# Kernel optimization log

Measured on AMD Instinct MI355X. Metric: run time of the kernel, lower is better.

The kernel has to match this reference:

```python
import jax, jax.numpy as jnp
import numpy as np

B, S, D, F, E, K, T = 4, 2048, 1024, 4096, 8, 2, 64


def setup_inputs() -> dict:
    key = jax.random.key(0)
    ks = jax.random.split(key, 12)
    s = 0.02
    return {
        "inputs": jax.random.normal(ks[0], (B, S, D), jnp.float32),
        "task_param": jax.random.normal(ks[1], (B, S, T), jnp.float32),
        "alpha": jnp.array(0.5, jnp.float32),
        "Wg_in": jax.random.normal(ks[2], (D, E), jnp.float32) * s,
        "bg_in": jnp.zeros((E,), jnp.float32),
        "Wg_task": jax.random.normal(ks[3], (T, E), jnp.float32) * s,
        "bg_task": jnp.zeros((E,), jnp.float32),
        "W1": jax.random.normal(ks[4], (E, D, F), jnp.float32) * s,
        "b1": jnp.zeros((E, F), jnp.float32),
        "W2": jax.random.normal(ks[5], (E, F, D), jnp.float32) * s,
        "b2": jnp.zeros((E, D), jnp.float32),
    }


def reference(inputs, task_param, alpha, Wg_in, bg_in, Wg_task, bg_task, W1, b1, W2, b2):
    dtype = inputs.dtype
    # blended gate logits: (1-alpha)*input_gate(x) + alpha*task_gate(task)
    gate_logits = (1.0 - alpha) * (jnp.einsum("bsd,de->bse", inputs, Wg_in) + bg_in) \
                + alpha * (jnp.einsum("bst,te->bse", task_param, Wg_task) + bg_task)
    # top-k expert selection (torch.topk: sorted descending)
    topk_vals, selected = jax.lax.top_k(gate_logits, K)  # [B,S,K]
    # aux load-balancing loss
    weights_softmax = jax.nn.softmax(gate_logits.astype(jnp.float32), axis=-1).astype(dtype)
    average_weight = weights_softmax.mean(axis=(0, 1))                 # [E]
    onehot = jax.nn.one_hot(selected, E, dtype=jnp.float32)            # [B,S,K,E]
    average_count = onehot.sum(axis=2).mean(axis=(0, 1)).astype(dtype) # [E]
    l_aux = jnp.mean(average_weight * average_count) * E
    # combine weights: softmax over the K selected logits, scattered to expert slots
    w = jax.nn.softmax(topk_vals.astype(jnp.float32), axis=-1).astype(dtype)  # [B,S,K]
    combine = jnp.einsum("bsk,bske->bse", w.astype(jnp.float32), onehot).astype(dtype)  # [B,S,E]
    # dense dispatch/combine (math-equivalent to boolean-mask gather/scatter loop)
    results = jnp.zeros_like(inputs)
    for e in range(E):
        h = jax.nn.gelu(jnp.einsum("bsd,df->bsf", inputs, W1[e]) + b1[e])
        y = jnp.einsum("bsf,fd->bsd", h, W2[e]) + b2[e]
        results = results + combine[..., e:e + 1] * y
    return (results, l_aux.astype(jnp.float32))
```

## Files before the change

kernel.cpp:

```cpp
#include <hip/hip_runtime.h>

#define NTOK 8192
#define DDIM 1024
#define FDIM 4096
#define NEXP 8
#define TDIM 64
#define MAXBLK 72

#define H_OFF   (1u<<20)
#define W1B_OFF (H_OFF + 134217728u)
#define W2B_OFF (W1B_OFF + 67108864u)
#define XB_OFF  (W2B_OFF + 67108864u)
#define FULL_WS (XB_OFF + 16777216u)
#define WS_BIG  (XB_OFF + 33554432u)

typedef __bf16 bf16x8 __attribute__((ext_vector_type(8)));
typedef unsigned short u16x8 __attribute__((ext_vector_type(8)));
typedef unsigned short u16x4 __attribute__((ext_vector_type(4)));
typedef float f32x4 __attribute__((ext_vector_type(4)));

__device__ __forceinline__ float gelu_tanh(float h) {
  float u = 0.7978845608028654f * (h + 0.044715f * h * h * h);
  float e = __expf(2.0f * u);
  return 0.5f * h * (2.0f - 2.0f / (e + 1.0f));
}

__device__ __forceinline__ void glds16(const void* g, void* l) {
  __builtin_amdgcn_global_load_lds((const __attribute__((address_space(1))) void*)g,
                                   (__attribute__((address_space(3))) void*)l, 16, 0, 0);
}

__global__ __launch_bounds__(256) void gate_kernel(
    const float* __restrict__ x, const float* __restrict__ task,
    const float* __restrict__ alpha_p,
    const float* __restrict__ Wg_in, const float* __restrict__ bg_in,
    const float* __restrict__ Wg_task, const float* __restrict__ bg_task,
    int* __restrict__ cnt, float* __restrict__ wsum,
    int* __restrict__ tok_list, float* __restrict__ wt_list)
{
  __shared__ float s_wsum[NEXP];
  int tid = threadIdx.x;
  if (tid < NEXP) s_wsum[tid] = 0.0f;
  __syncthreads();

  int lane = tid & 63;
  int wid  = tid >> 6;
  int tok  = blockIdx.x * 4 + wid;
  float a  = alpha_p[0];

  const float* xr = x + (size_t)tok * DDIM;
  float accd[8] = {0,0,0,0,0,0,0,0};
#pragma unroll
  for (int i = 0; i < DDIM/64; ++i) {
    int d = lane + 64*i;
    float xv = xr[d];
    f32x4 wa = *(const f32x4*)(Wg_in + (size_t)d*8);
    f32x4 wb = *(const f32x4*)(Wg_in + (size_t)d*8 + 4);
#pragma unroll
    for (int j = 0; j < 4; ++j) {
      accd[j]   = fmaf(xv, wa[j], accd[j]);
      accd[4+j] = fmaf(xv, wb[j], accd[4+j]);
    }
  }
  float part[8];
  {
    int d = lane;
    float tv = task[(size_t)tok*TDIM + d];
    f32x4 wa = *(const f32x4*)(Wg_task + (size_t)d*8);
    f32x4 wb = *(const f32x4*)(Wg_task + (size_t)d*8 + 4);
#pragma unroll
    for (int j = 0; j < 4; ++j) {
      part[j]   = (1.0f-a)*accd[j]   + a*(tv*wa[j]);
      part[4+j] = (1.0f-a)*accd[4+j] + a*(tv*wb[j]);
    }
  }
#pragma unroll
  for (int e = 0; e < 8; ++e) {
#pragma unroll
    for (int m = 1; m < 64; m <<= 1) part[e] += __shfl_xor(part[e], m);
  }

  if (lane == 0) {
    float lg[8];
#pragma unroll
    for (int e = 0; e < 8; ++e) lg[e] = part[e] + (1.0f-a)*bg_in[e] + a*bg_task[e];
    int e0 = 0;
#pragma unroll
    for (int e = 1; e < 8; ++e) if (lg[e] > lg[e0]) e0 = e;
    int e1 = (e0 == 0) ? 1 : 0;
#pragma unroll
    for (int e = 0; e < 8; ++e) if (e != e0 && lg[e] > lg[e1]) e1 = e;
    float mx = lg[0];
#pragma unroll
    for (int e = 1; e < 8; ++e) mx = fmaxf(mx, lg[e]);
    float p[8], s = 0.0f;
#pragma unroll
    for (int e = 0; e < 8; ++e) { p[e] = __expf(lg[e] - mx); s += p[e]; }
    float inv = 1.0f / s;
#pragma unroll
    for (int e = 0; e < 8; ++e) atomicAdd(&s_wsum[e], p[e] * inv);
    float p1 = __expf(lg[e1] - lg[e0]);
    float w0 = 1.0f / (1.0f + p1);
    float w1 = p1 * w0;
    int pos0 = atomicAdd(&cnt[e0], 1);
    tok_list[e0*NTOK + pos0] = tok; wt_list[e0*NTOK + pos0] = w0;
    int pos1 = atomicAdd(&cnt[e1], 1);
    tok_list[e1*NTOK + pos1] = tok; wt_list[e1*NTOK + pos1] = w1;
  }
  __syncthreads();
  if (tid < NEXP) atomicAdd(&wsum[tid], s_wsum[tid]);
}

__global__ void finalize_kernel(const int* __restrict__ cnt, const float* __restrict__ wsum,
                                int* __restrict__ offs, float* __restrict__ laux,
                                int* __restrict__ blk_e, int* __restrict__ blk_m)
{
  if (threadIdx.x == 0) {
    int o = 0; float l = 0.0f; int nb = 0;
    for (int e = 0; e < NEXP; ++e) {
      offs[e] = o;
      for (int m0 = 0; m0 < cnt[e]; m0 += 256) {
        if (nb < MAXBLK) { blk_e[nb] = e; blk_m[nb] = m0; ++nb; }
      }
      l += (wsum[e] * (1.0f/NTOK)) * ((float)cnt[e] * (1.0f/NTOK));
      o += cnt[e];
    }
    for (; nb < MAXBLK; ++nb) blk_e[nb] = -1;
    *laux = l;
  }
}

__global__ __launch_bounds__(256) void prep_x(const float* __restrict__ X,
                                              unsigned short* __restrict__ Xb)
{
  size_t i = ((size_t)blockIdx.x*256 + threadIdx.x)*8;
  f32x4 a = *(const f32x4*)(X + i);
  f32x4 b = *(const f32x4*)(X + i + 4);
  u16x8 v;
#pragma unroll
  for (int j = 0; j < 4; ++j) {
    v[j]   = __builtin_bit_cast(unsigned short, (__bf16)a[j]);
    v[4+j] = __builtin_bit_cast(unsigned short, (__bf16)b[j]);
  }
  *(u16x8*)(Xb + i) = v;
}

__global__ __launch_bounds__(256) void prep_gather(
    const float* __restrict__ X,
    const int* __restrict__ offs, const int* __restrict__ tok_list,
    unsigned short* __restrict__ Xg)
{
  int tid = threadIdx.x;
  int sl = blockIdx.x*2 + (tid >> 7);
  int e = 0;
#pragma unroll
  for (int k = 1; k < NEXP; ++k) if (sl >= offs[k]) e = k;
  int tok = tok_list[e*NTOK + (sl - offs[e])];
  int c8 = (tid & 127) * 8;
  const float* src = X + (size_t)tok * DDIM + c8;
  f32x4 a = *(const f32x4*)(src);
  f32x4 b = *(const f32x4*)(src + 4);
  u16x8 v;
#pragma unroll
  for (int j = 0; j < 4; ++j) {
    v[j]   = __builtin_bit_cast(unsigned short, (__bf16)a[j]);
    v[4+j] = __builtin_bit_cast(unsigned short, (__bf16)b[j]);
  }
  *(u16x8*)(Xg + (size_t)sl * DDIM + c8) = v;
}

template<bool PERM>
__global__ __launch_bounds__(256) void prep_w(const float* __restrict__ W,
                                              unsigned short* __restrict__ Wb,
                                              int N, int NKB, int NJ)
{
  int kb = blockIdx.x, J = blockIdx.y, e = blockIdx.z;
  int K = NKB*64;
  __shared__ unsigned short t[64*264];
  int tid = threadIdx.x;
  const float* src = W + ((size_t)e*K + (size_t)kb*64) * N + J*256;
  int k = tid >> 2, cg = tid & 3;
#pragma unroll
  for (int ii = 0; ii < 16; ++ii) {
    int n = cg*64 + ii*4;
    f32x4 v = *(const f32x4*)(src + (size_t)k*N + n);
    u16x4 b;
#pragma unroll
    for (int j = 0; j < 4; ++j) b[j] = __builtin_bit_cast(unsigned short, (__bf16)v[j]);
    *(u16x4*)&t[k*264 + n] = b;
  }
  __syncthreads();
  unsigned short* dst = Wb + ((size_t)(e*NJ + J)*NKB + kb)*16384;
#pragma unroll
  for (int i = 0; i < 8; ++i) {
    int c = i*256 + tid;
    int r = c >> 3, cc = c & 7;
    u16x8 v;
#pragma unroll
    for (int j = 0; j < 8; ++j) {
      int v64 = (cc ^ (r&7))*8 + j;
      int kl  = PERM ? (((v64 & 3) << 4) | (v64 >> 2)) : v64;
      v[j] = t[kl*264 + r];
    }
    *(u16x8*)(dst + c*8) = v;
  }
}


#define STAGE(sa, sb, ks) do {                                              \
  _Pragma("unroll")                                                         \
  for (int i_ = 0; i_ < 4; ++i_) {                                          \
    glds16(asrc[i_] + (size_t)(ks)*128, (char*)(sa) + dstoff[i_]);          \
    glds16(bsrc + (size_t)(ks)*32768 + i_*8192, (char*)(sb) + dstoff[i_]);  \
  }                                                                         \
} while (0)

#define COMPUTE(sa, sb) do {                                                \
  _Pragma("unroll")                                                         \
  for (int kk_ = 0; kk_ < 2; ++kk_) {                                       \
    int csw_ = ((kk_*4 + g) ^ (q & 7)) << 3;                                \
    bf16x8 bfv_[4];                                                         \
    _Pragma("unroll")                                                       \
    for (int ni_ = 0; ni_ < 4; ++ni_)                                       \
      bfv_[ni_] = *(const bf16x8*)&(sb)[(wc*64 + ni_*16 + q)*64 + csw_];    \
    _Pragma("unroll")                                                       \
    for (int mi_ = 0; mi_ < 8; ++mi_) {                                     \
      bf16x8 af_ = *(const bf16x8*)&(sa)[(wr*128 + mi_*16 + q)*64 + csw_];  \
      _Pragma("unroll")                                                     \
      for (int ni_ = 0; ni_ < 4; ++ni_)                                     \
        acc[mi_][ni_] = __builtin_amdgcn_mfma_f32_16x16x32_bf16(af_, bfv_[ni_], acc[mi_][ni_], 0, 0, 0); \
    }                                                                       \
  }                                                                         \
} while (0)

template<bool LIN>
__global__ __launch_bounds__(512) void gemm1_v8(
    const unsigned short* __restrict__ Xsrc, const unsigned short* __restrict__ W1b,
    const float* __restrict__ b1,
    const int* __restrict__ cnt, const int* __restrict__ offs,
    const int* __restrict__ tok_list,
    const int* __restrict__ blk_e, const int* __restrict__ blk_m,
    unsigned short* __restrict__ H)
{
  int e = blk_e[blockIdx.x];
  if (e < 0) return;
  int m0 = blk_m[blockIdx.x];
  int ce = cnt[e];
  int off = offs[e];
  int J = blockIdx.y;

  __shared__ __align__(16) unsigned short sA0[256*64], sB0[256*64];
  __shared__ __align__(16) unsigned short sA1[256*64], sB1[256*64];
  __shared__ int s_tok[256];

  int tid = threadIdx.x;
  if (!LIN) {
    if (tid < 256) {
      int idx = m0 + tid;
      s_tok[tid] = tok_list[e*NTOK + ((idx < ce) ? idx : (ce-1))];
    }
    __syncthreads();
  }

  int w = tid >> 6, l = tid & 63;
  int wr = w >> 2, wc = w & 3;
  int q = l & 15, g = l >> 4;

  const char* asrc[4];
  int dstoff[4];
#pragma unroll
  for (int i = 0; i < 4; ++i) {
    int c = i*512 + tid;
    int r = c >> 3, cc = c & 7;
    if (LIN) {
      int rr = (m0 + r < ce) ? r : (ce-1-m0);
      asrc[i] = (const char*)(Xsrc + (size_t)(off + m0 + rr)*DDIM) + ((cc ^ (r&7)) << 4);
    } else {
      asrc[i] = (const char*)(Xsrc + (size_t)s_tok[r]*DDIM) + ((cc ^ (r&7)) << 4);
    }
    dstoff[i] = c*16;
  }
  const char* bsrc = (const char*)W1b + ((size_t)(e*16 + J)*16)*32768 + (size_t)tid*16;

  f32x4 acc[8][4];
#pragma unroll
  for (int mi = 0; mi < 8; ++mi)
#pragma unroll
    for (int ni = 0; ni < 4; ++ni) acc[mi][ni] = (f32x4){0.f,0.f,0.f,0.f};

  STAGE(sA0, sB0, 0);
  asm volatile("s_waitcnt vmcnt(0)" ::: "memory");
  __builtin_amdgcn_s_barrier();

#define NK1 (DDIM/64)
  for (int ks = 0; ks < NK1; ks += 2) {
    STAGE(sA1, sB1, ks+1);
    COMPUTE(sA0, sB0);
    asm volatile("s_waitcnt vmcnt(0)" ::: "memory");
    __builtin_amdgcn_s_barrier();
    if (ks + 2 < NK1) STAGE(sA0, sB0, ks+2);
    COMPUTE(sA1, sB1);
    asm volatile("s_waitcnt vmcnt(0)" ::: "memory");
    __builtin_amdgcn_s_barrier();
  }

  int n0 = J*256;
  float bias[4];
#pragma unroll
  for (int ni = 0; ni < 4; ++ni) bias[ni] = b1[(size_t)e*FDIM + n0 + wc*64 + ni*16 + q];
#pragma unroll
  for (int mi = 0; mi < 8; ++mi) {
#pragma unroll
    for (int j = 0; j < 4; ++j) {
      int r = wr*128 + mi*16 + g*4 + j;
      if (m0 + r >= ce) continue;
      u16x4 hv;
#pragma unroll
      for (int ni = 0; ni < 4; ++ni) {
        float h = acc[mi][ni][j] + bias[ni];
        hv[ni] = __builtin_bit_cast(unsigned short, (__bf16)gelu_tanh(h));
      }
      *(u16x4*)&H[(size_t)(off + m0 + r)*FDIM + n0 + wc*64 + q*4] = hv;
    }
  }
}

__global__ __launch_bounds__(512) void gemm2_v8(
    const unsigned short* __restrict__ H, const unsigned short* __restrict__ W2b,
    const float* __restrict__ b2,
    const int* __restrict__ cnt, const int* __restrict__ offs,
    const int* __restrict__ tok_list, const float* __restrict__ wt_list,
    const int* __restrict__ blk_e, const int* __restrict__ blk_m,
    float* __restrict__ out)
{
  int e = blk_e[blockIdx.x];
  if (e < 0) return;
  int m0 = blk_m[blockIdx.x];
  int ce = cnt[e];
  int off = offs[e];
  int J = blockIdx.y;
  int s = blockIdx.z;

  __shared__ __align__(16) unsigned short sA0[256*64], sB0[256*64];
  __shared__ __align__(16) unsigned short sA1[256*64], sB1[256*64];
  __shared__ int   s_tok[256];
  __shared__ float s_wt[256];

  int tid = threadIdx.x;
  if (tid < 256) {
    int idx = m0 + tid;
    int cidx = (idx < ce) ? idx : (ce-1);
    s_tok[tid] = tok_list[e*NTOK + cidx];
    s_wt[tid]  = (idx < ce) ? wt_list[e*NTOK + cidx] : 0.0f;
  }
  __syncthreads();

  int w = tid >> 6, l = tid & 63;
  int wr = w >> 2, wc = w & 3;
  int q = l & 15, g = l >> 4;

  const char* asrc[4];
  int dstoff[4];
#pragma unroll
  for (int i = 0; i < 4; ++i) {
    int c = i*512 + tid;
    int r = c >> 3, cc = c & 7;
    int rr = (m0 + r < ce) ? r : (ce-1-m0);
    asrc[i]  = (const char*)(H + (size_t)(off + m0 + rr)*FDIM) + ((cc ^ (r&7)) << 4) + s*4096;
    dstoff[i] = c*16;
  }
  const char* bsrc = (const char*)W2b + ((size_t)(e*4 + J)*64 + s*32)*32768 + (size_t)tid*16;

  f32x4 acc[8][4];
#pragma unroll
  for (int mi = 0; mi < 8; ++mi)
#pragma unroll
    for (int ni = 0; ni < 4; ++ni) acc[mi][ni] = (f32x4){0.f,0.f,0.f,0.f};

  STAGE(sA0, sB0, 0);
  asm volatile("s_waitcnt vmcnt(0)" ::: "memory");
  __builtin_amdgcn_s_barrier();

#define NK2 (FDIM/64/2)
  for (int ks = 0; ks < NK2; ks += 2) {
    STAGE(sA1, sB1, ks+1);
    COMPUTE(sA0, sB0);
    asm volatile("s_waitcnt vmcnt(0)" ::: "memory");
    __builtin_amdgcn_s_barrier();
    if (ks + 2 < NK2) STAGE(sA0, sB0, ks+2);
    COMPUTE(sA1, sB1);
    asm volatile("s_waitcnt vmcnt(0)" ::: "memory");
    __builtin_amdgcn_s_barrier();
  }

  int n0 = J*256;
  float bias[4];
#pragma unroll
  for (int ni = 0; ni < 4; ++ni)
    bias[ni] = (s == 0) ? b2[(size_t)e*DDIM + n0 + wc*64 + ni*16 + q] : 0.0f;
#pragma unroll
  for (int mi = 0; mi < 8; ++mi) {
#pragma unroll
    for (int j = 0; j < 4; ++j) {
      int r = wr*128 + mi*16 + g*4 + j;
      if (m0 + r >= ce) continue;
      int tok = s_tok[r];
      float wt = s_wt[r];
      float* orow = out + (size_t)tok * DDIM;
#pragma unroll
      for (int ni = 0; ni < 4; ++ni) {
        float y = acc[mi][ni][j] + bias[ni];
        unsafeAtomicAdd(&orow[n0 + wc*64 + ni*16 + q], wt * y);
      }
    }
  }
}

extern "C" void kernel_launch(void* const* d_in, const int* in_sizes, int n_in,
                              void* d_out, int out_size, void* d_ws, size_t ws_size,
                              hipStream_t stream)
{
  const float* x       = (const float*)d_in[0];
  const float* task    = (const float*)d_in[1];
  const float* alpha   = (const float*)d_in[2];
  const float* Wg_in   = (const float*)d_in[3];
  const float* bg_in   = (const float*)d_in[4];
  const float* Wg_task = (const float*)d_in[5];
  const float* bg_task = (const float*)d_in[6];
  const float* W1      = (const float*)d_in[7];
  const float* b1      = (const float*)d_in[8];
  const float* W2      = (const float*)d_in[9];
  const float* b2      = (const float*)d_in[10];
  float* out = (float*)d_out;

  char* ws = (char*)d_ws;
  int*   cnt      = (int*)(ws + 0);
  float* wsum     = (float*)(ws + 32);
  int*   offs     = (int*)(ws + 64);
  int*   blk_e    = (int*)(ws + 128);
  int*   blk_m    = (int*)(ws + 512);
  int*   tok_list = (int*)(ws + 4096);
  float* wt_list  = (float*)(ws + 4096 + NTOK*NEXP*4);
  unsigned short* H   = (unsigned short*)(ws + H_OFF);
  unsigned short* W1b = (unsigned short*)(ws + W1B_OFF);
  unsigned short* W2b = (unsigned short*)(ws + W2B_OFF);
  unsigned short* Xb  = (unsigned short*)(ws + XB_OFF);
  unsigned short* Xg  = (unsigned short*)(ws + XB_OFF);

  hipMemsetAsync(d_out, 0, (size_t)out_size * sizeof(float), stream);
  hipMemsetAsync(ws, 0, 128, stream);
  gate_kernel<<<NTOK/4, 256, 0, stream>>>(x, task, alpha, Wg_in, bg_in, Wg_task, bg_task,
                                          cnt, wsum, tok_list, wt_list);
  finalize_kernel<<<1, 64, 0, stream>>>(cnt, wsum, offs, out + (size_t)NTOK*DDIM, blk_e, blk_m);
  prep_w<false><<<dim3(16, 16, NEXP), 256, 0, stream>>>(W1, W1b, FDIM, 16, 16);
  prep_w<true ><<<dim3(64,  4, NEXP), 256, 0, stream>>>(W2, W2b, DDIM, 64, 4);

  if (ws_size >= (size_t)WS_BIG) {
    prep_gather<<<NTOK, 256, 0, stream>>>(x, offs, tok_list, Xg);
    gemm1_v8<true><<<dim3(MAXBLK, FDIM/256), 512, 0, stream>>>(Xg, W1b, b1, cnt, offs,
                                                               tok_list, blk_e, blk_m, H);
  } else {
    prep_x<<<NTOK*DDIM/2048, 256, 0, stream>>>(x, Xb);
    gemm1_v8<false><<<dim3(MAXBLK, FDIM/256), 512, 0, stream>>>(Xb, W1b, b1, cnt, offs,
                                                                tok_list, blk_e, blk_m, H);
  }
  gemm2_v8<<<dim3(MAXBLK, DDIM/256, 2), 512, 0, stream>>>(H, W2b, b2, cnt, offs, tok_list,
                                                          wt_list, blk_e, blk_m, out);
}
```

Baseline: 850.0 us.

## Pre-tile gathered activations and H into swizzled contiguous tiles for GEMMs

Adds a gather kernel that writes the per-expert token rows of X as bf16 into tile-contiguous, pre-swizzled 256x64 blocks, one group per routing block. gemm1 then writes its GELU output H in the same tiled layout, so both GEMMs stage A and B with fully contiguous 16-byte loads at a fixed offset per k-step instead of strided per-row addresses. The goal is fewer scattered global reads and less address arithmetic in the staging loop. In exchange it needs a larger workspace, padded per block, and keeps the old row-major path only as a fallback.

After: 858.7 us. Within noise of the previous version (+1.0%).

```diff
diff --git a/kernel.cpp b/kernel.cpp
--- a/kernel.cpp
+++ b/kernel.cpp
@@ -7,12 +7,16 @@
 #define TDIM 64
 #define MAXBLK 72
 
-#define H_OFF   (1u<<20)
-#define W1B_OFF (H_OFF + 134217728u)
-#define W2B_OFF (W1B_OFF + 67108864u)
-#define XB_OFF  (W2B_OFF + 67108864u)
-#define FULL_WS (XB_OFF + 16777216u)
-#define WS_BIG  (XB_OFF + 33554432u)
+#define HG_OFF   1048576u
+#define W1B_OFF  (HG_OFF + 150994944u)
+#define W2B_OFF  (W1B_OFF + 67108864u)
+#define XGT_OFF  (W2B_OFF + 67108864u)
+#define WS_NEED  (XGT_OFF + 37748736u)
+#define FB_H     1048576u
+#define FB_W1B   (FB_H + 134217728u)
+#define FB_W2B   (FB_W1B + 67108864u)
+#define FB_XB    (FB_W2B + 67108864u)
+#define FB_NEED  (FB_XB + 16777216u)
 
 typedef __bf16 bf16x8 __attribute__((ext_vector_type(8)));
 typedef unsigned short u16x8 __attribute__((ext_vector_type(8)));
@@ -130,45 +134,6 @@
   }
 }
 
-__global__ __launch_bounds__(256) void prep_x(const float* __restrict__ X,
-                                              unsigned short* __restrict__ Xb)
-{
-  size_t i = ((size_t)blockIdx.x*256 + threadIdx.x)*8;
-  f32x4 a = *(const f32x4*)(X + i);
-  f32x4 b = *(const f32x4*)(X + i + 4);
-  u16x8 v;
-#pragma unroll
-  for (int j = 0; j < 4; ++j) {
-    v[j]   = __builtin_bit_cast(unsigned short, (__bf16)a[j]);
-    v[4+j] = __builtin_bit_cast(unsigned short, (__bf16)b[j]);
-  }
-  *(u16x8*)(Xb + i) = v;
-}
-
-__global__ __launch_bounds__(256) void prep_gather(
-    const float* __restrict__ X,
-    const int* __restrict__ offs, const int* __restrict__ tok_list,
-    unsigned short* __restrict__ Xg)
-{
-  int tid = threadIdx.x;
-  int sl = blockIdx.x*2 + (tid >> 7);
-  int e = 0;
-#pragma unroll
-  for (int k = 1; k < NEXP; ++k) if (sl >= offs[k]) e = k;
-  int tok = tok_list[e*NTOK + (sl - offs[e])];
-  int c8 = (tid & 127) * 8;
-  const float* src = X + (size_t)tok * DDIM + c8;
-  f32x4 a = *(const f32x4*)(src);
-  f32x4 b = *(const f32x4*)(src + 4);
-  u16x8 v;
-#pragma unroll
-  for (int j = 0; j < 4; ++j) {
-    v[j]   = __builtin_bit_cast(unsigned short, (__bf16)a[j]);
-    v[4+j] = __builtin_bit_cast(unsigned short, (__bf16)b[j]);
-  }
-  *(u16x8*)(Xg + (size_t)sl * DDIM + c8) = v;
-}
-
 template<bool PERM>
 __global__ __launch_bounds__(256) void prep_w(const float* __restrict__ W,
                                               unsigned short* __restrict__ Wb,
@@ -206,12 +171,48 @@
   }
 }
 
+__global__ __launch_bounds__(256) void prep_gather_t(
+    const float* __restrict__ X,
+    const int* __restrict__ cnt, const int* __restrict__ tok_list,
+    const int* __restrict__ blk_e, const int* __restrict__ blk_m,
+    unsigned short* __restrict__ XgT)
+{
+  int kt = blockIdx.x, bi = blockIdx.y;
+  int e = blk_e[bi];
+  if (e < 0) return;
+  int m0 = blk_m[bi], ce = cnt[e];
+  __shared__ int s_tok[256];
+  int tid = threadIdx.x;
+  if (tid < 256) {
+    int idx = m0 + tid;
+    s_tok[tid] = tok_list[e*NTOK + ((idx < ce) ? idx : (ce-1))];
+  }
+  __syncthreads();
+  unsigned short* dst = XgT + ((size_t)bi*16 + kt)*16384;
+#pragma unroll
+  for (int i = 0; i < 8; ++i) {
+    int c = i*256 + tid;
+    int r = c >> 3, cc = c & 7;
+    int d = cc ^ (r & 7);
+    const float* src = X + (size_t)s_tok[r]*DDIM + kt*64 + d*8;
+    f32x4 a = *(const f32x4*)(src);
+    f32x4 b = *(const f32x4*)(src + 4);
+    u16x8 v;
+#pragma unroll
+    for (int j = 0; j < 4; ++j) {
+      v[j]   = __builtin_bit_cast(unsigned short, (__bf16)a[j]);
+      v[4+j] = __builtin_bit_cast(unsigned short, (__bf16)b[j]);
+    }
+    *(u16x8*)(dst + (size_t)c*8) = v;
+  }
+}
+
 
 #define STAGE(sa, sb, ks) do {                                              \
   _Pragma("unroll")                                                         \
   for (int i_ = 0; i_ < 4; ++i_) {                                          \
-    glds16(asrc[i_] + (size_t)(ks)*128, (char*)(sa) + dstoff[i_]);          \
-    glds16(bsrc + (size_t)(ks)*32768 + i_*8192, (char*)(sb) + dstoff[i_]);  \
+    glds16(abase + (size_t)(ks)*32768 + dstoff[i_], (char*)(sa) + dstoff[i_]); \
+    glds16(bbase + (size_t)(ks)*32768 + dstoff[i_], (char*)(sb) + dstoff[i_]); \
   }                                                                         \
 } while (0)
 
@@ -233,18 +234,200 @@
   }                                                                         \
 } while (0)
 
-template<bool LIN>
-__global__ __launch_bounds__(512) void gemm1_v8(
-    const unsigned short* __restrict__ Xsrc, const unsigned short* __restrict__ W1b,
+__global__ __launch_bounds__(512) void gemm1_v9(
+    const unsigned short* __restrict__ XgT, const unsigned short* __restrict__ W1b,
+    const float* __restrict__ b1,
+    const int* __restrict__ cnt,
+    const int* __restrict__ blk_e, const int* __restrict__ blk_m,
+    unsigned short* __restrict__ Hg)
+{
+  int bi = blockIdx.x;
+  int e = blk_e[bi];
+  if (e < 0) return;
+  int m0 = blk_m[bi];
+  int ce = cnt[e];
+  int J = blockIdx.y;
+
+  __shared__ __align__(16) unsigned short sA0[256*64], sB0[256*64];
+  __shared__ __align__(16) unsigned short sA1[256*64], sB1[256*64];
+
+  int tid = threadIdx.x;
+  int w = tid >> 6, l = tid & 63;
+  int wr = w >> 2, wc = w & 3;
+  int q = l & 15, g = l >> 4;
+
+  int dstoff[4];
+#pragma unroll
+  for (int i = 0; i < 4; ++i) dstoff[i] = i*8192 + tid*16;
+  const char* abase = (const char*)XgT + (size_t)bi*524288;
+  const char* bbase = (const char*)W1b + ((size_t)(e*16 + J)*16)*32768;
+
+  f32x4 acc[8][4];
+#pragma unroll
+  for (int mi = 0; mi < 8; ++mi)
+#pragma unroll
+    for (int ni = 0; ni < 4; ++ni) acc[mi][ni] = (f32x4){0.f,0.f,0.f,0.f};
+
+  STAGE(sA0, sB0, 0);
+  asm volatile("s_waitcnt vmcnt(0)" ::: "memory");
+  __builtin_amdgcn_s_barrier();
+
+#define NK1 (DDIM/64)
+  for (int ks = 0; ks < NK1; ks += 2) {
+    STAGE(sA1, sB1, ks+1);
+    COMPUTE(sA0, sB0);
+    asm volatile("s_waitcnt vmcnt(0)" ::: "memory");
+    __builtin_amdgcn_s_barrier();
+    if (ks + 2 < NK1) STAGE(sA0, sB0, ks+2);
+    COMPUTE(sA1, sB1);
+    asm volatile("s_waitcnt vmcnt(0)" ::: "memory");
+    __builtin_amdgcn_s_barrier();
+  }
+
+  int J4wc = J*4 + wc;
+  unsigned short* hgb = Hg + (((size_t)bi*2 + (J4wc >> 5))*32 + (J4wc & 31))*16384;
+  int n0 = J*256;
+  float bias[4];
+#pragma unroll
+  for (int ni = 0; ni < 4; ++ni) bias[ni] = b1[(size_t)e*FDIM + n0 + wc*64 + ni*16 + q];
+#pragma unroll
+  for (int mi = 0; mi < 8; ++mi) {
+#pragma unroll
+    for (int j = 0; j < 4; ++j) {
+      int r = wr*128 + mi*16 + g*4 + j;
+      if (m0 + r >= ce) continue;
+      u16x4 hv;
+#pragma unroll
+      for (int ni = 0; ni < 4; ++ni) {
+        float h = acc[mi][ni][j] + bias[ni];
+        hv[ni] = __builtin_bit_cast(unsigned short, (__bf16)gelu_tanh(h));
+      }
+      int cc = (q >> 1) ^ (r & 7);
+      *(u16x4*)&hgb[(r*8 + cc)*8 + (q & 1)*4] = hv;
+    }
+  }
+}
+
+__global__ __launch_bounds__(512) void gemm2_v9(
+    const unsigned short* __restrict__ Hg, const unsigned short* __restrict__ W2b,
+    const float* __restrict__ b2,
+    const int* __restrict__ cnt, const int* __restrict__ offs,
+    const int* __restrict__ tok_list, const float* __restrict__ wt_list,
+    const int* __restrict__ blk_e, const int* __restrict__ blk_m,
+    float* __restrict__ out)
+{
+  int bi = blockIdx.x;
+  int e = blk_e[bi];
+  if (e < 0) return;
+  int m0 = blk_m[bi];
+  int ce = cnt[e];
+  int J = blockIdx.y;
+  int s = blockIdx.z;
+
+  __shared__ __align__(16) unsigned short sA0[256*64], sB0[256*64];
+  __shared__ __align__(16) unsigned short sA1[256*64], sB1[256*64];
+  __shared__ int   s_tok[256];
+  __shared__ float s_wt[256];
+
+  int tid = threadIdx.x;
+  if (tid < 256) {
+    int idx = m0 + tid;
+    int cidx = (idx < ce) ? idx : (ce-1);
+    s_tok[tid] = tok_list[e*NTOK + cidx];
+    s_wt[tid]  = (idx < ce) ? wt_list[e*NTOK + cidx] : 0.0f;
+  }
+  __syncthreads();
+
+  int w = tid >> 6, l = tid & 63;
+  int wr = w >> 2, wc = w & 3;
+  int q = l & 15, g = l >> 4;
+
+  int dstoff[4];
+#pragma unroll
+  for (int i = 0; i < 4; ++i) dstoff[i] = i*8192 + tid*16;
+  const char* abase = (const char*)Hg + (((size_t)bi*2 + s)*32)*32768;
+  const char* bbase = (const char*)W2b + ((size_t)(e*4 + J)*64 + s*32)*32768;
+
+  f32x4 acc[8][4];
+#pragma unroll
+  for (int mi = 0; mi < 8; ++mi)
+#pragma unroll
+    for (int ni = 0; ni < 4; ++ni) acc[mi][ni] = (f32x4){0.f,0.f,0.f,0.f};
+
+  STAGE(sA0, sB0, 0);
+  asm volatile("s_waitcnt vmcnt(0)" ::: "memory");
+  __builtin_amdgcn_s_barrier();
+
+#define NK2 (FDIM/64/2)
+  for (int ks = 0; ks < NK2; ks += 2) {
+    STAGE(sA1, sB1, ks+1);
+    COMPUTE(sA0, sB0);
+    asm volatile("s_waitcnt vmcnt(0)" ::: "memory");
+    __builtin_amdgcn_s_barrier();
+    if (ks + 2 < NK2) STAGE(sA0, sB0, ks+2);
+    COMPUTE(sA1, sB1);
+    asm volatile("s_waitcnt vmcnt(0)" ::: "memory");
+    __builtin_amdgcn_s_barrier();
+  }
+
+  int n0 = J*256;
+  float bias[4];
+#pragma unroll
+  for (int ni = 0; ni < 4; ++ni)
+    bias[ni] = (s == 0) ? b2[(size_t)e*DDIM + n0 + wc*64 + ni*16 + q] : 0.0f;
+#pragma unroll
+  for (int mi = 0; mi < 8; ++mi) {
+#pragma unroll
+    for (int j = 0; j < 4; ++j) {
+      int r = wr*128 + mi*16 + g*4 + j;
+      if (m0 + r >= ce) continue;
+      int tok = s_tok[r];
+      float wt = s_wt[r];
+      float* orow = out + (size_t)tok * DDIM;
+#pragma unroll
+      for (int ni = 0; ni < 4; ++ni) {
+        float y = acc[mi][ni][j] + bias[ni];
+        unsafeAtomicAdd(&orow[n0 + wc*64 + ni*16 + q], wt * y);
+      }
+    }
+  }
+}
+
+__global__ __launch_bounds__(256) void prep_x(const float* __restrict__ X,
+                                              unsigned short* __restrict__ Xb)
+{
+  size_t i = ((size_t)blockIdx.x*256 + threadIdx.x)*8;
+  f32x4 a = *(const f32x4*)(X + i);
+  f32x4 b = *(const f32x4*)(X + i + 4);
+  u16x8 v;
+#pragma unroll
+  for (int j = 0; j < 4; ++j) {
+    v[j]   = __builtin_bit_cast(unsigned short, (__bf16)a[j]);
+    v[4+j] = __builtin_bit_cast(unsigned short, (__bf16)b[j]);
+  }
+  *(u16x8*)(Xb + i) = v;
+}
+
+#define STAGE_FB(sa, sb, ks) do {                                           \
+  _Pragma("unroll")                                                         \
+  for (int i_ = 0; i_ < 4; ++i_) {                                          \
+    glds16(asrc[i_] + (size_t)(ks)*128, (char*)(sa) + dstoff[i_]);          \
+    glds16(bbase + (size_t)(ks)*32768 + dstoff[i_], (char*)(sb) + dstoff[i_]); \
+  }                                                                         \
+} while (0)
+
+__global__ __launch_bounds__(512) void gemm1_fb(
+    const unsigned short* __restrict__ Xb, const unsigned short* __restrict__ W1b,
     const float* __restrict__ b1,
     const int* __restrict__ cnt, const int* __restrict__ offs,
     const int* __restrict__ tok_list,
     const int* __restrict__ blk_e, const int* __restrict__ blk_m,
     unsigned short* __restrict__ H)
 {
-  int e = blk_e[blockIdx.x];
+  int bi = blockIdx.x;
+  int e = blk_e[bi];
   if (e < 0) return;
-  int m0 = blk_m[blockIdx.x];
+  int m0 = blk_m[bi];
   int ce = cnt[e];
   int off = offs[e];
   int J = blockIdx.y;
@@ -254,13 +437,11 @@
   __shared__ int s_tok[256];
 
   int tid = threadIdx.x;
-  if (!LIN) {
-    if (tid < 256) {
-      int idx = m0 + tid;
-      s_tok[tid] = tok_list[e*NTOK + ((idx < ce) ? idx : (ce-1))];
-    }
-    __syncthreads();
-  }
+  if (tid < 256) {
+    int idx = m0 + tid;
+    s_tok[tid] = tok_list[e*NTOK + ((idx < ce) ? idx : (ce-1))];
+  }
+  __syncthreads();
 
   int w = tid >> 6, l = tid & 63;
   int wr = w >> 2, wc = w & 3;
@@ -272,15 +453,10 @@
   for (int i = 0; i < 4; ++i) {
     int c = i*512 + tid;
     int r = c >> 3, cc = c & 7;
-    if (LIN) {
-      int rr = (m0 + r < ce) ? r : (ce-1-m0);
-      asrc[i] = (const char*)(Xsrc + (size_t)(off + m0 + rr)*DDIM) + ((cc ^ (r&7)) << 4);
-    } else {
-      asrc[i] = (const char*)(Xsrc + (size_t)s_tok[r]*DDIM) + ((cc ^ (r&7)) << 4);
-    }
+    asrc[i] = (const char*)(Xb + (size_t)s_tok[r]*DDIM) + ((cc ^ (r&7)) << 4);
     dstoff[i] = c*16;
   }
-  const char* bsrc = (const char*)W1b + ((size_t)(e*16 + J)*16)*32768 + (size_t)tid*16;
+  const char* bbase = (const char*)W1b + ((size_t)(e*16 + J)*16)*32768;
 
   f32x4 acc[8][4];
 #pragma unroll
@@ -288,17 +464,16 @@
 #pragma unroll
     for (int ni = 0; ni < 4; ++ni) acc[mi][ni] = (f32x4){0.f,0.f,0.f,0.f};
 
-  STAGE(sA0, sB0, 0);
+  STAGE_FB(sA0, sB0, 0);
   asm volatile("s_waitcnt vmcnt(0)" ::: "memory");
   __builtin_amdgcn_s_barrier();
 
-#define NK1 (DDIM/64)
   for (int ks = 0; ks < NK1; ks += 2) {
-    STAGE(sA1, sB1, ks+1);
+    STAGE_FB(sA1, sB1, ks+1);
     COMPUTE(sA0, sB0);
     asm volatile("s_waitcnt vmcnt(0)" ::: "memory");
     __builtin_amdgcn_s_barrier();
-    if (ks + 2 < NK1) STAGE(sA0, sB0, ks+2);
+    if (ks + 2 < NK1) STAGE_FB(sA0, sB0, ks+2);
     COMPUTE(sA1, sB1);
     asm volatile("s_waitcnt vmcnt(0)" ::: "memory");
     __builtin_amdgcn_s_barrier();
@@ -325,7 +500,7 @@
   }
 }
 
-__global__ __launch_bounds__(512) void gemm2_v8(
+__global__ __launch_bounds__(512) void gemm2_fb(
     const unsigned short* __restrict__ H, const unsigned short* __restrict__ W2b,
     const float* __restrict__ b2,
     const int* __restrict__ cnt, const int* __restrict__ offs,
@@ -333,9 +508,10 @@
     const int* __restrict__ blk_e, const int* __restrict__ blk_m,
     float* __restrict__ out)
 {
-  int e = blk_e[blockIdx.x];
+  int bi = blockIdx.x;
+  int e = blk_e[bi];
   if (e < 0) return;
-  int m0 = blk_m[blockIdx.x];
+  int m0 = blk_m[bi];
   int ce = cnt[e];
   int off = offs[e];
   int J = blockIdx.y;
@@ -369,7 +545,7 @@
     asrc[i]  = (const char*)(H + (size_t)(off + m0 + rr)*FDIM) + ((cc ^ (r&7)) << 4) + s*4096;
     dstoff[i] = c*16;
   }
-  const char* bsrc = (const char*)W2b + ((size_t)(e*4 + J)*64 + s*32)*32768 + (size_t)tid*16;
+  const char* bbase = (const char*)W2b + ((size_t)(e*4 + J)*64 + s*32)*32768;
 
   f32x4 acc[8][4];
 #pragma unroll
@@ -377,17 +553,16 @@
 #pragma unroll
     for (int ni = 0; ni < 4; ++ni) acc[mi][ni] = (f32x4){0.f,0.f,0.f,0.f};
 
-  STAGE(sA0, sB0, 0);
+  STAGE_FB(sA0, sB0, 0);
   asm volatile("s_waitcnt vmcnt(0)" ::: "memory");
   __builtin_amdgcn_s_barrier();
 
-#define NK2 (FDIM/64/2)
   for (int ks = 0; ks < NK2; ks += 2) {
-    STAGE(sA1, sB1, ks+1);
+    STAGE_FB(sA1, sB1, ks+1);
     COMPUTE(sA0, sB0);
     asm volatile("s_waitcnt vmcnt(0)" ::: "memory");
     __builtin_amdgcn_s_barrier();
-    if (ks + 2 < NK2) STAGE(sA0, sB0, ks+2);
+    if (ks + 2 < NK2) STAGE_FB(sA0, sB0, ks+2);
     COMPUTE(sA1, sB1);
     asm volatile("s_waitcnt vmcnt(0)" ::: "memory");
     __builtin_amdgcn_s_barrier();
@@ -441,29 +616,35 @@
   int*   blk_m    = (int*)(ws + 512);
   int*   tok_list = (int*)(ws + 4096);
   float* wt_list  = (float*)(ws + 4096 + NTOK*NEXP*4);
-  unsigned short* H   = (unsigned short*)(ws + H_OFF);
-  unsigned short* W1b = (unsigned short*)(ws + W1B_OFF);
-  unsigned short* W2b = (unsigned short*)(ws + W2B_OFF);
-  unsigned short* Xb  = (unsigned short*)(ws + XB_OFF);
-  unsigned short* Xg  = (unsigned short*)(ws + XB_OFF);
 
   hipMemsetAsync(d_out, 0, (size_t)out_size * sizeof(float), stream);
   hipMemsetAsync(ws, 0, 128, stream);
   gate_kernel<<<NTOK/4, 256, 0, stream>>>(x, task, alpha, Wg_in, bg_in, Wg_task, bg_task,
                                           cnt, wsum, tok_list, wt_list);
   finalize_kernel<<<1, 64, 0, stream>>>(cnt, wsum, offs, out + (size_t)NTOK*DDIM, blk_e, blk_m);
-  prep_w<false><<<dim3(16, 16, NEXP), 256, 0, stream>>>(W1, W1b, FDIM, 16, 16);
-  prep_w<true ><<<dim3(64,  4, NEXP), 256, 0, stream>>>(W2, W2b, DDIM, 64, 4);
-
-  if (ws_size >= (size_t)WS_BIG) {
-    prep_gather<<<NTOK, 256, 0, stream>>>(x, offs, tok_list, Xg);
-    gemm1_v8<true><<<dim3(MAXBLK, FDIM/256), 512, 0, stream>>>(Xg, W1b, b1, cnt, offs,
-                                                               tok_list, blk_e, blk_m, H);
+
+  if (ws_size >= (size_t)WS_NEED) {
+    unsigned short* Hg  = (unsigned short*)(ws + HG_OFF);
+    unsigned short* W1b = (unsigned short*)(ws + W1B_OFF);
+    unsigned short* W2b = (unsigned short*)(ws + W2B_OFF);
+    unsigned short* XgT = (unsigned short*)(ws + XGT_OFF);
+    prep_w<false><<<dim3(16, 16, NEXP), 256, 0, stream>>>(W1, W1b, FDIM, 16, 16);
+    prep_w<true ><<<dim3(64,  4, NEXP), 256, 0, stream>>>(W2, W2b, DDIM, 64, 4);
+    prep_gather_t<<<dim3(16, MAXBLK), 256, 0, stream>>>(x, cnt, tok_list, blk_e, blk_m, XgT);
+    gemm1_v9<<<dim3(MAXBLK, FDIM/256), 512, 0, stream>>>(XgT, W1b, b1, cnt, blk_e, blk_m, Hg);
+    gemm2_v9<<<dim3(MAXBLK, DDIM/256, 2), 512, 0, stream>>>(Hg, W2b, b2, cnt, offs, tok_list,
+                                                            wt_list, blk_e, blk_m, out);
   } else {
+    unsigned short* H   = (unsigned short*)(ws + FB_H);
+    unsigned short* W1b = (unsigned short*)(ws + FB_W1B);
+    unsigned short* W2b = (unsigned short*)(ws + FB_W2B);
+    unsigned short* Xb  = (unsigned short*)(ws + FB_XB);
+    prep_w<false><<<dim3(16, 16, NEXP), 256, 0, stream>>>(W1, W1b, FDIM, 16, 16);
+    prep_w<true ><<<dim3(64,  4, NEXP), 256, 0, stream>>>(W2, W2b, DDIM, 64, 4);
     prep_x<<<NTOK*DDIM/2048, 256, 0, stream>>>(x, Xb);
-    gemm1_v8<false><<<dim3(MAXBLK, FDIM/256), 512, 0, stream>>>(Xb, W1b, b1, cnt, offs,
-                                                                tok_list, blk_e, blk_m, H);
-  }
-  gemm2_v8<<<dim3(MAXBLK, DDIM/256, 2), 512, 0, stream>>>(H, W2b, b2, cnt, offs, tok_list,
-                                                          wt_list, blk_e, blk_m, out);
-}
+    gemm1_fb<<<dim3(MAXBLK, FDIM/256), 512, 0, stream>>>(Xb, W1b, b1, cnt, offs, tok_list,
+                                                         blk_e, blk_m, H);
+    gemm2_fb<<<dim3(MAXBLK, DDIM/256, 2), 512, 0, stream>>>(H, W2b, b2, cnt, offs, tok_list,
+                                                            wt_list, blk_e, blk_m, out);
+  }
+}
```
